# Performance work log

Hardware: AMD Instinct MI355X
Metric: run time of the kernel (lower is better)

## Reference

```python
import jax, jax.numpy as jnp
import numpy as np
from jax import lax

V, E, H, K, T, B = 32000, 512, 512, 32, 256, 64
PAD_W = 0          # word_dict['PAD']
START, END, PAD_L = 30, 31, 0   # label_dict
NEG = -100000.0


def setup_inputs() -> dict:
    key = jax.random.key(0)
    ks = jax.random.split(key, 12)
    s = 1.0 / np.sqrt(H)
    tokens = jax.random.randint(ks[0], (T, B), 1, V, dtype=jnp.int32)   # >PAD_W -> mask all ones
    tags = jax.random.randint(ks[1], (T, B), 1, K - 2, dtype=jnp.int32)
    lengths = jnp.full((B,), T, dtype=jnp.int32)
    embed = jax.random.normal(ks[2], (V, E), jnp.float32) * 0.1
    wih0 = jax.random.uniform(ks[3], (2, 4 * H, E), jnp.float32, -s, s)
    whh0 = jax.random.uniform(ks[4], (2, 4 * H, H), jnp.float32, -s, s)
    b0 = jax.random.uniform(ks[5], (2, 4 * H), jnp.float32, -s, s)
    wih1 = jax.random.uniform(ks[6], (2, 4 * H, 2 * H), jnp.float32, -s, s)
    whh1 = jax.random.uniform(ks[7], (2, 4 * H, H), jnp.float32, -s, s)
    b1 = jax.random.uniform(ks[8], (2, 4 * H), jnp.float32, -s, s)
    lin_w = jax.random.uniform(ks[9], (K, 2 * H), jnp.float32, -s, s)
    lin_b = jax.random.uniform(ks[10], (K,), jnp.float32, -s, s)
    trans = jax.random.normal(ks[11], (K, K), jnp.float32)
    # replicate the torch transition init (same order of assignments)
    trans = trans.at[START, :].set(NEG)
    trans = trans.at[:, END].set(NEG)
    trans = trans.at[:, PAD_L].set(NEG)
    trans = trans.at[PAD_L, :].set(NEG)
    trans = trans.at[PAD_L, END].set(0.0)
    trans = trans.at[PAD_L, PAD_L].set(0.0)
    return dict(tokens=tokens, tags=tags, lengths=lengths, embed=embed,
                wih0=wih0, whh0=whh0, b0=b0, wih1=wih1, whh1=whh1, b1=b1,
                lin_w=lin_w, lin_b=lin_b, trans=trans)


def _lstm_dir(x, w_ih, w_hh, b, reverse):
    # x: [T,B,in] -> hs: [T,B,H]; gates precomputed as one big GEMM
    xp = jnp.einsum('tbi,gi->tbg', x, w_ih) + b  # [T,B,4H]
    h0 = jnp.zeros((x.shape[1], H), x.dtype)

    def step(carry, g_in):
        h, c = carry
        g = g_in + h @ w_hh.T
        i, f, gg, o = jnp.split(g, 4, axis=-1)  # torch gate order i,f,g,o
        c = jax.nn.sigmoid(f) * c + jax.nn.sigmoid(i) * jnp.tanh(gg)
        h = jax.nn.sigmoid(o) * jnp.tanh(c)
        return (h, c), h

    _, hs = lax.scan(step, (h0, h0), xp, reverse=reverse)
    return hs


def _bilstm_layer(x, wih, whh, b):
    return jnp.concatenate([_lstm_dir(x, wih[0], whh[0], b[0], False),
                            _lstm_dir(x, wih[1], whh[1], b[1], True)], axis=-1)


def reference(tokens, tags, lengths, embed, wih0, whh0, b0, wih1, whh1, b1,
              lin_w, lin_b, trans):
    mask = (tokens > PAD_W).astype(jnp.float32)  # [T,B]
    x = embed[tokens]                            # [T,B,E]
    x = _bilstm_layer(x, wih0, whh0, b0)
    x = _bilstm_layer(x, wih1, whh1, b1)
    feats = x @ lin_w.T + lin_b                  # [T,B,K]

    nB = tokens.shape[1]
    # ---- CRF forward algorithm: log Z(x) ----
    init = jnp.full((nB, K), NEG, feats.dtype).at[:, START].set(0.0)

    def step(score, inp):
        emit, m = inp  # [B,K], [B]
        # new[b,k] = logsumexp_j(score[b,j] + trans[k,j]) + emit[b,k]
        new = jax.nn.logsumexp(score[:, None, :] + trans[None, :, :], axis=2) + emit
        return jnp.where(m[:, None] > 0, new, score), None

    z, _ = lax.scan(step, init, (feats, mask))
    log_z = jax.nn.logsumexp(z + trans[END][None, :], axis=1)  # [B]

    # ---- gold path score (vectorized, masked deltas sum) ----
    start_row = jnp.full((1, nB), START, dtype=tags.dtype)
    te = jnp.concatenate([start_row, tags], axis=0)            # [T+1,B]
    trans_s = trans[te[1:], te[:-1]]                           # [T,B]
    emit_s = jnp.take_along_axis(feats, te[1:][..., None].astype(jnp.int32), axis=2)[..., 0]
    gold = jnp.sum(mask * (trans_s + emit_s), axis=0) + trans[END, te[-1]]

    return jnp.sum((log_z - gold) / lengths.astype(jnp.float32))
```

## Files before the change

kernel.cpp:

```cpp
#include <hip/hip_runtime.h>
#include <math.h>

#define T_STEPS 256
#define BATCH   64
#define HID     512
#define KTAGS   32
#define NEGV    -100000.0f
#define START_TAG 30
#define END_TAG   31

#define NBLK      256
#define SPIN_LIM  (1 << 24)
#define LAYER_DONE  300u
#define POISON_DONE 301u
#define POISON    0xFFFFFFFFFFFFFFFFULL

typedef __attribute__((ext_vector_type(8))) short short8;
typedef __attribute__((ext_vector_type(4))) float f32x4;

union V16 { uint4 u; short8 s; };
union HQ  { unsigned long long q[2]; short8 s; };

static __device__ __forceinline__ unsigned short f2b(float f) {
    unsigned u = __float_as_uint(f);
    return (unsigned short)((u + 0x7fffu + ((u >> 16) & 1u)) >> 16);
}
static __device__ __forceinline__ float b2f(unsigned short us) {
    return __uint_as_float(((unsigned)us) << 16);
}

__global__ __launch_bounds__(256) void init_zero(unsigned int* __restrict__ flags,
                                                 unsigned long long* __restrict__ hbuf,
                                                 float* __restrict__ out)
{
    int i = blockIdx.x * 256 + threadIdx.x;
    if (i < 131072)
        __hip_atomic_store(hbuf + i, POISON, __ATOMIC_RELAXED, __HIP_MEMORY_SCOPE_AGENT);
    if (i < 16384)
        __hip_atomic_store(flags + i, 0u, __ATOMIC_RELAXED, __HIP_MEMORY_SCOPE_AGENT);
    if (i == 0)
        __hip_atomic_store(out, 0.0f, __ATOMIC_RELAXED, __HIP_MEMORY_SCOPE_AGENT);
}

__global__ __launch_bounds__(256) void convert_embed(const float* __restrict__ src,
                                                     unsigned short* __restrict__ dst)
{
    long long i = ((long long)blockIdx.x * 256 + threadIdx.x) * 4;
    if (i >= (long long)32000 * 512) return;
    float4 v = *(const float4*)(src + i);
    ushort4 o;
    o.x = f2b(v.x); o.y = f2b(v.y); o.z = f2b(v.z); o.w = f2b(v.w);
    *(ushort4*)(dst + i) = o;
}

__global__ __launch_bounds__(256) void pack_w(const float* __restrict__ wih,
                                              const float* __restrict__ whh,
                                              int xK,
                                              unsigned short* __restrict__ wpack)
{
    const int xKt = xK >> 5, KT = xKt + 16;
    long long t = (long long)blockIdx.x * 256 + threadIdx.x;
    if (t >= (long long)2 * 64 * KT * 2 * 64) return;
    int lane = (int)(t & 63);
    long long rest = t >> 6;
    int nf = (int)(rest & 1); rest >>= 1;
    int kt = (int)(rest % KT); rest /= KT;
    int nt = (int)(rest % 64);
    int d  = (int)(rest / 64);
    int c = lane & 15, q = lane >> 4;
    int bc = nf * 16 + c;
    int r = (bc >> 3) * 512 + nt * 8 + (bc & 7);
    const float* src;
    if (kt < xKt) src = wih + ((long long)d * 2048 * xK + (long long)r * xK + kt * 32 + q * 8);
    else          src = whh + ((long long)d * 2048 * 512 + (long long)r * 512 + (kt - xKt) * 32 + q * 8);
    float4 v0 = *(const float4*)src;
    float4 v1 = *(const float4*)(src + 4);
    unsigned short o[8] = { f2b(v0.x), f2b(v0.y), f2b(v0.z), f2b(v0.w),
                            f2b(v1.x), f2b(v1.y), f2b(v1.z), f2b(v1.w) };
    *(uint4*)(wpack + t * 8) = *(const uint4*)o;
}

template<int XK>
static __device__ __forceinline__ void layer_steps(
    const int d, const int bg, const int nt, const int tid,
    const int* __restrict__ tokens,
    const unsigned short* __restrict__ embB,
    const unsigned short* __restrict__ hs_in,
    const unsigned short* __restrict__ wp,
    const float* __restrict__ bia,
    unsigned short* __restrict__ hso,
    unsigned long long* __restrict__ hbuf64,
    uint4* __restrict__ wlds,
    float (&Gred)[2][4][32][36])
{
    constexpr bool L0  = (XK == 512);
    constexpr int  xKt = XK >> 5;
    constexpr int  KT  = xKt + 16;
    constexpr int  nX  = xKt >> 2;

    const int w = tid >> 6, lane = tid & 63;
    const int lm = lane & 15, q = lane >> 4;
    const int brow = tid >> 3, hc = tid & 7;

    const uint4* wp4 = (const uint4*)wp;
    for (int j = tid; j < KT * 128; j += 256)
        wlds[j] = wp4[j];

    float breg[4];
    #pragma unroll
    for (int g = 0; g < 4; ++g) breg[g] = bia[g * 512 + nt * 8 + hc];
    float creg = 0.0f;

    __syncthreads();

    for (int s = 0; s < T_STEPS; ++s) {
        const int tt = d ? (T_STEPS - 1 - s) : s;
        const int p  = s & 1;

        const unsigned short* xr[2];
        #pragma unroll
        for (int mt = 0; mt < 2; ++mt) {
            int m = mt * 16 + lm;
            if (L0) {
                int tok = tokens[tt * BATCH + bg * 32 + m];
                xr[mt] = embB + (long long)tok * 512;
            } else {
                xr[mt] = hs_in + ((long long)tt * 64 + bg * 32 + m) * 1024;
            }
        }

        uint4 av[nX][2];
        #pragma unroll
        for (int i = 0; i < nX; ++i) {
            const int kt = w * nX + i;
            #pragma unroll
            for (int mt = 0; mt < 2; ++mt)
                av[i][mt] = *(const uint4*)(xr[mt] + kt * 32 + q * 8);
        }

        HQ hq[4][2];
        const unsigned long long* hbq =
            hbuf64 + (long long)(((((s - 1) & 7) * 2 + d) * 2 + bg)) * 4096;
        if (s > 0) {
            #pragma unroll
            for (int i = 0; i < 4; ++i) {
                const int kth = w * 4 + i;
                #pragma unroll
                for (int mt = 0; mt < 2; ++mt) {
                    const int base = (kth * 4 + q) * 64 + (mt * 16 + lm) * 2;
                    hq[i][mt].q[0] = __hip_atomic_load(hbq + base,     __ATOMIC_RELAXED, __HIP_MEMORY_SCOPE_AGENT);
                    hq[i][mt].q[1] = __hip_atomic_load(hbq + base + 1, __ATOMIC_RELAXED, __HIP_MEMORY_SCOPE_AGENT);
                }
            }
        }

        f32x4 acc[2][2];
        #pragma unroll
        for (int mt = 0; mt < 2; ++mt)
            #pragma unroll
            for (int nf = 0; nf < 2; ++nf) acc[mt][nf] = (f32x4)0.0f;

        #pragma unroll
        for (int i = 0; i < nX; ++i) {
            const int kt = w * nX + i;
            V16 a0, a1, b0, b1;
            a0.u = av[i][0]; a1.u = av[i][1];
            b0.u = wlds[(kt * 2 + 0) * 64 + lane];
            b1.u = wlds[(kt * 2 + 1) * 64 + lane];
            acc[0][0] = __builtin_amdgcn_mfma_f32_16x16x32_bf16(a0.s, b0.s, acc[0][0], 0, 0, 0);
            acc[0][1] = __builtin_amdgcn_mfma_f32_16x16x32_bf16(a0.s, b1.s, acc[0][1], 0, 0, 0);
            acc[1][0] = __builtin_amdgcn_mfma_f32_16x16x32_bf16(a1.s, b0.s, acc[1][0], 0, 0, 0);
            acc[1][1] = __builtin_amdgcn_mfma_f32_16x16x32_bf16(a1.s, b1.s, acc[1][1], 0, 0, 0);
        }

        if (s > 0) {
            int pass = 0;
            for (;;) {
                int ok = 1;
                #pragma unroll
                for (int i = 0; i < 4; ++i)
                    #pragma unroll
                    for (int mt = 0; mt < 2; ++mt)
                        ok &= (hq[i][mt].q[0] != POISON) && (hq[i][mt].q[1] != POISON);
                if (__all(ok)) break;
                if (++pass > SPIN_LIM) break;
                if (pass >= 3) __builtin_amdgcn_s_sleep(1);
                #pragma unroll
                for (int i = 0; i < 4; ++i) {
                    const int kth = w * 4 + i;
                    #pragma unroll
                    for (int mt = 0; mt < 2; ++mt) {
                        const int base = (kth * 4 + q) * 64 + (mt * 16 + lm) * 2;
                        hq[i][mt].q[0] = __hip_atomic_load(hbq + base,     __ATOMIC_RELAXED, __HIP_MEMORY_SCOPE_AGENT);
                        hq[i][mt].q[1] = __hip_atomic_load(hbq + base + 1, __ATOMIC_RELAXED, __HIP_MEMORY_SCOPE_AGENT);
                    }
                }
            }

            #pragma unroll
            for (int i = 0; i < 4; ++i) {
                const int kth = w * 4 + i;
                V16 b0, b1;
                b0.u = wlds[((xKt + kth) * 2 + 0) * 64 + lane];
                b1.u = wlds[((xKt + kth) * 2 + 1) * 64 + lane];
                acc[0][0] = __builtin_amdgcn_mfma_f32_16x16x32_bf16(hq[i][0].s, b0.s, acc[0][0], 0, 0, 0);
                acc[0][1] = __builtin_amdgcn_mfma_f32_16x16x32_bf16(hq[i][0].s, b1.s, acc[0][1], 0, 0, 0);
                acc[1][0] = __builtin_amdgcn_mfma_f32_16x16x32_bf16(hq[i][1].s, b0.s, acc[1][0], 0, 0, 0);
                acc[1][1] = __builtin_amdgcn_mfma_f32_16x16x32_bf16(hq[i][1].s, b1.s, acc[1][1], 0, 0, 0);
            }
        }

        #pragma unroll
        for (int mt = 0; mt < 2; ++mt)
            #pragma unroll
            for (int nf = 0; nf < 2; ++nf)
                #pragma unroll
                for (int r = 0; r < 4; ++r) {
                    const int row = mt * 16 + q * 4 + r;
                    const int c   = nf * 16 + lm;
                    const int cp  = (c & 7) * 4 + (c >> 3);
                    Gred[p][w][row][cp] = acc[mt][nf][r];
                }
        __syncthreads();

        float vg[4];
        {
            const float4 g0 = *(const float4*)&Gred[p][0][brow][hc * 4];
            const float4 g1 = *(const float4*)&Gred[p][1][brow][hc * 4];
            const float4 g2 = *(const float4*)&Gred[p][2][brow][hc * 4];
            const float4 g3 = *(const float4*)&Gred[p][3][brow][hc * 4];
            vg[0] = breg[0] + g0.x + g1.x + g2.x + g3.x;
            vg[1] = breg[1] + g0.y + g1.y + g2.y + g3.y;
            vg[2] = breg[2] + g0.z + g1.z + g2.z + g3.z;
            vg[3] = breg[3] + g0.w + g1.w + g2.w + g3.w;
        }
        const float si = 1.0f / (1.0f + __expf(-vg[0]));
        const float sf = 1.0f / (1.0f + __expf(-vg[1]));
        const float so = 1.0f / (1.0f + __expf(-vg[3]));
        const float cn = sf * creg + si * tanhf(vg[2]);
        const float hn = so * tanhf(cn);
        creg = cn;

        unsigned pv = (unsigned)f2b(hn);
        unsigned p2 = pv | (__shfl_xor(pv, 1) << 16);
        unsigned long long hv = (unsigned long long)p2
                              | ((unsigned long long)__shfl_xor(p2, 2) << 32);
        if ((tid & 3) == 0) {
            const int row = brow, cq = hc >> 2;
            unsigned long long* dst =
                hbuf64 + ((long long)((((s & 7) * 2 + d) * 2 + bg) * 64 + nt)) * 64 + row * 2 + cq;
            __hip_atomic_store(dst, hv, __ATOMIC_RELAXED, __HIP_MEMORY_SCOPE_AGENT);
            *(unsigned long long*)(hso + ((long long)tt * 64 + bg * 32 + row) * 1024
                                       + d * 512 + nt * 8 + cq * 4) = hv;
            unsigned long long* pdst =
                hbuf64 + ((long long)(((((s + 2) & 7) * 2 + d) * 2 + bg) * 64 + nt)) * 64 + row * 2 + cq;
            __hip_atomic_store(pdst, POISON, __ATOMIC_RELAXED, __HIP_MEMORY_SCOPE_AGENT);
        }
    }
}

__global__ __launch_bounds__(256, 1) void lstm_mfma(
    const int* __restrict__ tokens,
    const unsigned short* __restrict__ embB,
    const unsigned short* __restrict__ wp0,
    const unsigned short* __restrict__ wp1,
    const float* __restrict__ bb0, const float* __restrict__ bb1,
    unsigned short* __restrict__ hs0,
    unsigned short* __restrict__ hs1,
    unsigned long long* __restrict__ hbuf64,
    unsigned int* __restrict__ flags)
{
    __shared__ uint4 wlds[6144];
    __shared__ __align__(16) float Gred[2][4][32][36];

    const int bid = blockIdx.x;
    const int d   = bid >> 7;
    const int bg  = (bid >> 6) & 1;
    const int nt  = bid & 63;
    const int tid = threadIdx.x;

    layer_steps<512>(d, bg, nt, tid, tokens, embB, (const unsigned short*)nullptr,
                     wp0 + (long long)(d * 64 + nt) * 32 * 1024,
                     bb0 + (long long)d * 2048,
                     hs0, hbuf64, wlds, Gred);

    {
        __threadfence();
        __syncthreads();
        if (tid == 0)
            __hip_atomic_store(flags + bid * 32, LAYER_DONE,
                               __ATOMIC_RELAXED, __HIP_MEMORY_SCOPE_AGENT);
        if (tid < 64) {
            int n = 0;
            for (;;) {
                unsigned a = __hip_atomic_load(flags + tid * 32,         __ATOMIC_RELAXED, __HIP_MEMORY_SCOPE_AGENT);
                unsigned b = __hip_atomic_load(flags + (tid + 64) * 32,  __ATOMIC_RELAXED, __HIP_MEMORY_SCOPE_AGENT);
                unsigned c = __hip_atomic_load(flags + (tid + 128) * 32, __ATOMIC_RELAXED, __HIP_MEMORY_SCOPE_AGENT);
                unsigned e = __hip_atomic_load(flags + (tid + 192) * 32, __ATOMIC_RELAXED, __HIP_MEMORY_SCOPE_AGENT);
                if (__all(a >= LAYER_DONE && b >= LAYER_DONE &&
                          c >= LAYER_DONE && e >= LAYER_DONE)) break;
                __builtin_amdgcn_s_sleep(1);
                if (++n > SPIN_LIM) break;
            }
        }
        __syncthreads();
        if (tid < 64) {
            #pragma unroll
            for (int pp = 0; pp < 8; ++pp) {
                unsigned long long* pd =
                    hbuf64 + ((long long)(((pp * 2 + d) * 2 + bg) * 64 + nt)) * 64 + tid;
                __hip_atomic_store(pd, POISON, __ATOMIC_RELAXED, __HIP_MEMORY_SCOPE_AGENT);
            }
        }
        asm volatile("s_waitcnt vmcnt(0)" ::: "memory");
        __syncthreads();
        if (tid == 0)
            __hip_atomic_store(flags + bid * 32, POISON_DONE,
                               __ATOMIC_RELAXED, __HIP_MEMORY_SCOPE_AGENT);
        if (tid < 64) {
            int n = 0;
            for (;;) {
                unsigned a = __hip_atomic_load(flags + tid * 32,         __ATOMIC_RELAXED, __HIP_MEMORY_SCOPE_AGENT);
                unsigned b = __hip_atomic_load(flags + (tid + 64) * 32,  __ATOMIC_RELAXED, __HIP_MEMORY_SCOPE_AGENT);
                unsigned c = __hip_atomic_load(flags + (tid + 128) * 32, __ATOMIC_RELAXED, __HIP_MEMORY_SCOPE_AGENT);
                unsigned e = __hip_atomic_load(flags + (tid + 192) * 32, __ATOMIC_RELAXED, __HIP_MEMORY_SCOPE_AGENT);
                if (__all(a >= POISON_DONE && b >= POISON_DONE &&
                          c >= POISON_DONE && e >= POISON_DONE)) break;
                __builtin_amdgcn_s_sleep(1);
                if (++n > SPIN_LIM) break;
            }
        }
        __syncthreads();
        __threadfence();
    }

    layer_steps<1024>(d, bg, nt, tid, tokens, embB, hs0,
                      wp1 + (long long)(d * 64 + nt) * 48 * 1024,
                      bb1 + (long long)d * 2048,
                      hs1, hbuf64, wlds, Gred);
}

__global__ __launch_bounds__(256) void gemm_feats(
    const unsigned short* __restrict__ A,
    const float* __restrict__ W,
    const float* __restrict__ bias,
    float* __restrict__ C,
    int M, int N, int K)
{
    __shared__ __align__(16) float As[64][34];
    __shared__ __align__(16) float Ws[32][68];

    const int m0 = blockIdx.y * 64;
    const int tid = threadIdx.x;
    const int tr = tid >> 4;
    const int tc = tid & 15;

    float acc[4][4];
    #pragma unroll
    for (int i = 0; i < 4; ++i)
        #pragma unroll
        for (int j = 0; j < 4; ++j) acc[i][j] = 0.0f;

    for (int k0 = 0; k0 < K; k0 += 32) {
        {
            int row = tid >> 2, g8 = tid & 3;
            uint4 v = *(const uint4*)(A + ((long long)(m0 + row)) * 1024 + k0 + g8 * 8);
            const unsigned short* pv = (const unsigned short*)&v;
            #pragma unroll
            for (int e = 0; e < 8; ++e) As[row][g8 * 8 + e] = b2f(pv[e]);
        }
        {
            int row = tid >> 3, q2 = tid & 7;
            float4 v = *(const float4*)(W + (long long)row * K + k0 + 4 * q2);
            Ws[4*q2+0][row] = v.x; Ws[4*q2+1][row] = v.y;
            Ws[4*q2+2][row] = v.z; Ws[4*q2+3][row] = v.w;
        }
        __syncthreads();
        #pragma unroll 8
        for (int kk = 0; kk < 32; ++kk) {
            float a0 = As[4*tr+0][kk], a1 = As[4*tr+1][kk];
            float a2 = As[4*tr+2][kk], a3 = As[4*tr+3][kk];
            float4 wv = *(const float4*)&Ws[kk][4*tc];
            acc[0][0] += a0*wv.x; acc[0][1] += a0*wv.y; acc[0][2] += a0*wv.z; acc[0][3] += a0*wv.w;
            acc[1][0] += a1*wv.x; acc[1][1] += a1*wv.y; acc[1][2] += a1*wv.z; acc[1][3] += a1*wv.w;
            acc[2][0] += a2*wv.x; acc[2][1] += a2*wv.y; acc[2][2] += a2*wv.z; acc[2][3] += a2*wv.w;
            acc[3][0] += a3*wv.x; acc[3][1] += a3*wv.y; acc[3][2] += a3*wv.z; acc[3][3] += a3*wv.w;
        }
        __syncthreads();
    }
    #pragma unroll
    for (int i = 0; i < 4; ++i) {
        int m = m0 + 4*tr + i;
        #pragma unroll
        for (int j = 0; j < 4; ++j) {
            int n = 4*tc + j;
            if (n < N) C[(long long)m * N + n] = acc[i][j] + bias[n];
        }
    }
}

__global__ __launch_bounds__(1024) void crf_kernel(
    const float* __restrict__ feats,
    const float* __restrict__ trans,
    const int*   __restrict__ tokens,
    const int*   __restrict__ tags,
    const int*   __restrict__ lengths,
    float* __restrict__ out)
{
    const int b = blockIdx.x;
    const int tid = threadIdx.x;
    __shared__ float tr_s[KTAGS*KTAGS];
    __shared__ float score_s[KTAGS];
    __shared__ float emit_s[KTAGS];
    __shared__ float red_s[16];
    __shared__ float logz_s;

    tr_s[tid] = trans[tid];
    if (tid < KTAGS) score_s[tid] = (tid == START_TAG) ? 0.0f : NEGV;
    __syncthreads();

    const int i = tid >> 5, j = tid & 31;
    for (int t = 0; t < T_STEPS; ++t) {
        if (tid < KTAGS) emit_s[tid] = feats[((long long)t*BATCH + b)*KTAGS + tid];
        __syncthreads();
        float e = score_s[j] + tr_s[i*KTAGS + j];
        float m = e;
        m = fmaxf(m, __shfl_xor(m, 1));  m = fmaxf(m, __shfl_xor(m, 2));
        m = fmaxf(m, __shfl_xor(m, 4));  m = fmaxf(m, __shfl_xor(m, 8));
        m = fmaxf(m, __shfl_xor(m, 16));
        float p = __expf(e - m);
        p += __shfl_xor(p, 1); p += __shfl_xor(p, 2); p += __shfl_xor(p, 4);
        p += __shfl_xor(p, 8); p += __shfl_xor(p, 16);
        float nv = m + __logf(p) + emit_s[i];
        int msk = tokens[(long long)t*BATCH + b] > 0;
        __syncthreads();
        if (j == 0) score_s[i] = msk ? nv : score_s[i];
        __syncthreads();
    }

    if (tid < KTAGS) {
        float v = score_s[tid] + tr_s[END_TAG*KTAGS + tid];
        float m = v;
        m = fmaxf(m, __shfl_xor(m, 1));  m = fmaxf(m, __shfl_xor(m, 2));
        m = fmaxf(m, __shfl_xor(m, 4));  m = fmaxf(m, __shfl_xor(m, 8));
        m = fmaxf(m, __shfl_xor(m, 16));
        float p = __expf(v - m);
        p += __shfl_xor(p, 1); p += __shfl_xor(p, 2); p += __shfl_xor(p, 4);
        p += __shfl_xor(p, 8); p += __shfl_xor(p, 16);
        if (tid == 0) logz_s = m + __logf(p);
    }
    __syncthreads();

    float val = 0.0f;
    if (tid < T_STEPS) {
        int t = tid;
        int cur  = tags[(long long)t*BATCH + b];
        int prev = (t == 0) ? START_TAG : tags[(long long)(t-1)*BATCH + b];
        int msk  = tokens[(long long)t*BATCH + b] > 0;
        if (msk) val = tr_s[cur*KTAGS + prev]
                     + feats[((long long)t*BATCH + b)*KTAGS + cur];
    }
    val += __shfl_xor(val, 1);  val += __shfl_xor(val, 2);
    val += __shfl_xor(val, 4);  val += __shfl_xor(val, 8);
    val += __shfl_xor(val, 16); val += __shfl_xor(val, 32);
    int wave = tid >> 6, lane = tid & 63;
    if (lane == 0) red_s[wave] = val;
    __syncthreads();
    if (tid == 0) {
        float g = 0.0f;
        #pragma unroll
        for (int w = 0; w < 16; ++w) g += red_s[w];
        g += tr_s[END_TAG*KTAGS + tags[(long long)(T_STEPS-1)*BATCH + b]];
        atomicAdd(out, (logz_s - g) / (float)lengths[b]);
    }
}

extern "C" void kernel_launch(void* const* d_in, const int* in_sizes, int n_in,
                              void* d_out, int out_size, void* d_ws, size_t ws_size,
                              hipStream_t stream) {
    const int*   tokens  = (const int*)  d_in[0];
    const int*   tags    = (const int*)  d_in[1];
    const int*   lengths = (const int*)  d_in[2];
    const float* embed   = (const float*)d_in[3];
    const float* wih0    = (const float*)d_in[4];
    const float* whh0    = (const float*)d_in[5];
    const float* b0      = (const float*)d_in[6];
    const float* wih1    = (const float*)d_in[7];
    const float* whh1    = (const float*)d_in[8];
    const float* b1      = (const float*)d_in[9];
    const float* lin_w   = (const float*)d_in[10];
    const float* lin_b   = (const float*)d_in[11];
    const float* trans   = (const float*)d_in[12];

    char* ws = (char*)d_ws;
    unsigned short* hs0   = (unsigned short*)(ws);
    unsigned short* hs1   = (unsigned short*)(ws +  33554432ULL);
    unsigned short* embB  = (unsigned short*)(ws +  67108864ULL);
    unsigned short* wp0   = (unsigned short*)(ws +  99876864ULL);
    unsigned short* wp1   = (unsigned short*)(ws + 108265472ULL);
    float*          feats = (float*)        (ws + 120848384ULL);
    unsigned int*   flagsP = (unsigned int*)feats;
    unsigned long long* hbufP = (unsigned long long*)((char*)feats + 65536);

    float* out = (float*)d_out;

    init_zero<<<dim3(512), 256, 0, stream>>>(flagsP, hbufP, out);
    convert_embed<<<dim3(16000), 256, 0, stream>>>(embed, embB);
    pack_w<<<dim3(2048), 256, 0, stream>>>(wih0, whh0, 512,  wp0);
    pack_w<<<dim3(3072), 256, 0, stream>>>(wih1, whh1, 1024, wp1);

    lstm_mfma<<<dim3(NBLK), 256, 0, stream>>>(
        tokens, embB, wp0, wp1, b0, b1, hs0, hs1, hbufP, flagsP);

    gemm_feats<<<dim3(1, 256, 1), 256, 0, stream>>>(
        hs1, lin_w, lin_b, feats, T_STEPS*BATCH, KTAGS, 2*HID);

    crf_kernel<<<dim3(BATCH), 1024, 0, stream>>>(feats, trans, tokens, tags,
                                                 lengths, out);
}
```

Measured before the change: 2.312 ms.

## Process both batch halves per block, halving persistent LSTM grid size

```diff
diff --git a/kernel.cpp b/kernel.cpp
--- a/kernel.cpp
+++ b/kernel.cpp
@@ -9,7 +9,7 @@
 #define START_TAG 30
 #define END_TAG   31
 
-#define NBLK      256
+#define NBLK      128
 #define SPIN_LIM  (1 << 24)
 #define LAYER_DONE  300u
 #define POISON_DONE 301u
@@ -82,7 +82,7 @@
 
 template<int XK>
 static __device__ __forceinline__ void layer_steps(
-    const int d, const int bg, const int nt, const int tid,
+    const int d, const int nt, const int tid,
     const int* __restrict__ tokens,
     const unsigned short* __restrict__ embB,
     const unsigned short* __restrict__ hs_in,
@@ -109,38 +109,32 @@
     float breg[4];
     #pragma unroll
     for (int g = 0; g < 4; ++g) breg[g] = bia[g * 512 + nt * 8 + hc];
-    float creg = 0.0f;
+    float creg0 = 0.0f, creg1 = 0.0f;
 
     __syncthreads();
 
     for (int s = 0; s < T_STEPS; ++s) {
         const int tt = d ? (T_STEPS - 1 - s) : s;
-        const int p  = s & 1;
-
-        const unsigned short* xr[2];
+
+        const unsigned short* xr0[2];
         #pragma unroll
         for (int mt = 0; mt < 2; ++mt) {
             int m = mt * 16 + lm;
-            if (L0) {
-                int tok = tokens[tt * BATCH + bg * 32 + m];
-                xr[mt] = embB + (long long)tok * 512;
-            } else {
-                xr[mt] = hs_in + ((long long)tt * 64 + bg * 32 + m) * 1024;
-            }
-        }
-
-        uint4 av[nX][2];
+            if (L0) xr0[mt] = embB + (long long)tokens[tt * BATCH + m] * 512;
+            else    xr0[mt] = hs_in + ((long long)tt * 64 + m) * 1024;
+        }
+        uint4 av0[nX][2];
         #pragma unroll
         for (int i = 0; i < nX; ++i) {
             const int kt = w * nX + i;
             #pragma unroll
             for (int mt = 0; mt < 2; ++mt)
-                av[i][mt] = *(const uint4*)(xr[mt] + kt * 32 + q * 8);
-        }
-
-        HQ hq[4][2];
-        const unsigned long long* hbq =
-            hbuf64 + (long long)(((((s - 1) & 7) * 2 + d) * 2 + bg)) * 4096;
+                av0[i][mt] = *(const uint4*)(xr0[mt] + kt * 32 + q * 8);
+        }
+
+        HQ hq0[4][2];
+        const unsigned long long* hbq0 =
+            hbuf64 + (long long)((((s - 1) & 7) * 2 + d) * 2 + 0) * 4096;
         if (s > 0) {
             #pragma unroll
             for (int i = 0; i < 4; ++i) {
@@ -148,8 +142,8 @@
                 #pragma unroll
                 for (int mt = 0; mt < 2; ++mt) {
                     const int base = (kth * 4 + q) * 64 + (mt * 16 + lm) * 2;
-                    hq[i][mt].q[0] = __hip_atomic_load(hbq + base,     __ATOMIC_RELAXED, __HIP_MEMORY_SCOPE_AGENT);
-                    hq[i][mt].q[1] = __hip_atomic_load(hbq + base + 1, __ATOMIC_RELAXED, __HIP_MEMORY_SCOPE_AGENT);
+                    hq0[i][mt].q[0] = __hip_atomic_load(hbq0 + base,     __ATOMIC_RELAXED, __HIP_MEMORY_SCOPE_AGENT);
+                    hq0[i][mt].q[1] = __hip_atomic_load(hbq0 + base + 1, __ATOMIC_RELAXED, __HIP_MEMORY_SCOPE_AGENT);
                 }
             }
         }
@@ -164,7 +158,7 @@
         for (int i = 0; i < nX; ++i) {
             const int kt = w * nX + i;
             V16 a0, a1, b0, b1;
-            a0.u = av[i][0]; a1.u = av[i][1];
+            a0.u = av0[i][0]; a1.u = av0[i][1];
             b0.u = wlds[(kt * 2 + 0) * 64 + lane];
             b1.u = wlds[(kt * 2 + 1) * 64 + lane];
             acc[0][0] = __builtin_amdgcn_mfma_f32_16x16x32_bf16(a0.s, b0.s, acc[0][0], 0, 0, 0);
@@ -173,6 +167,37 @@
             acc[1][1] = __builtin_amdgcn_mfma_f32_16x16x32_bf16(a1.s, b1.s, acc[1][1], 0, 0, 0);
         }
 
+        const unsigned short* xr1[2];
+        #pragma unroll
+        for (int mt = 0; mt < 2; ++mt) {
+            int m = mt * 16 + lm;
+            if (L0) xr1[mt] = embB + (long long)tokens[tt * BATCH + 32 + m] * 512;
+            else    xr1[mt] = hs_in + ((long long)tt * 64 + 32 + m) * 1024;
+        }
+        uint4 av1[nX][2];
+        #pragma unroll
+        for (int i = 0; i < nX; ++i) {
+            const int kt = w * nX + i;
+            #pragma unroll
+            for (int mt = 0; mt < 2; ++mt)
+                av1[i][mt] = *(const uint4*)(xr1[mt] + kt * 32 + q * 8);
+        }
+        HQ hq1[4][2];
+        const unsigned long long* hbq1 =
+            hbuf64 + (long long)((((s - 1) & 7) * 2 + d) * 2 + 1) * 4096;
+        if (s > 0) {
+            #pragma unroll
+            for (int i = 0; i < 4; ++i) {
+                const int kth = w * 4 + i;
+                #pragma unroll
+                for (int mt = 0; mt < 2; ++mt) {
+                    const int base = (kth * 4 + q) * 64 + (mt * 16 + lm) * 2;
+                    hq1[i][mt].q[0] = __hip_atomic_load(hbq1 + base,     __ATOMIC_RELAXED, __HIP_MEMORY_SCOPE_AGENT);
+                    hq1[i][mt].q[1] = __hip_atomic_load(hbq1 + base + 1, __ATOMIC_RELAXED, __HIP_MEMORY_SCOPE_AGENT);
+                }
+            }
+        }
+
         if (s > 0) {
             int pass = 0;
             for (;;) {
@@ -181,7 +206,7 @@
                 for (int i = 0; i < 4; ++i)
                     #pragma unroll
                     for (int mt = 0; mt < 2; ++mt)
-                        ok &= (hq[i][mt].q[0] != POISON) && (hq[i][mt].q[1] != POISON);
+                        ok &= (hq0[i][mt].q[0] != POISON) && (hq0[i][mt].q[1] != POISON);
                 if (__all(ok)) break;
                 if (++pass > SPIN_LIM) break;
                 if (pass >= 3) __builtin_amdgcn_s_sleep(1);
@@ -191,22 +216,21 @@
                     #pragma unroll
                     for (int mt = 0; mt < 2; ++mt) {
                         const int base = (kth * 4 + q) * 64 + (mt * 16 + lm) * 2;
-                        hq[i][mt].q[0] = __hip_atomic_load(hbq + base,     __ATOMIC_RELAXED, __HIP_MEMORY_SCOPE_AGENT);
-                        hq[i][mt].q[1] = __hip_atomic_load(hbq + base + 1, __ATOMIC_RELAXED, __HIP_MEMORY_SCOPE_AGENT);
+                        hq0[i][mt].q[0] = __hip_atomic_load(hbq0 + base,     __ATOMIC_RELAXED, __HIP_MEMORY_SCOPE_AGENT);
+                        hq0[i][mt].q[1] = __hip_atomic_load(hbq0 + base + 1, __ATOMIC_RELAXED, __HIP_MEMORY_SCOPE_AGENT);
                     }
                 }
             }
-
             #pragma unroll
             for (int i = 0; i < 4; ++i) {
                 const int kth = w * 4 + i;
                 V16 b0, b1;
                 b0.u = wlds[((xKt + kth) * 2 + 0) * 64 + lane];
                 b1.u = wlds[((xKt + kth) * 2 + 1) * 64 + lane];
-                acc[0][0] = __builtin_amdgcn_mfma_f32_16x16x32_bf16(hq[i][0].s, b0.s, acc[0][0], 0, 0, 0);
-                acc[0][1] = __builtin_amdgcn_mfma_f32_16x16x32_bf16(hq[i][0].s, b1.s, acc[0][1], 0, 0, 0);
-                acc[1][0] = __builtin_amdgcn_mfma_f32_16x16x32_bf16(hq[i][1].s, b0.s, acc[1][0], 0, 0, 0);
-                acc[1][1] = __builtin_amdgcn_mfma_f32_16x16x32_bf16(hq[i][1].s, b1.s, acc[1][1], 0, 0, 0);
+                acc[0][0] = __builtin_amdgcn_mfma_f32_16x16x32_bf16(hq0[i][0].s, b0.s, acc[0][0], 0, 0, 0);
+                acc[0][1] = __builtin_amdgcn_mfma_f32_16x16x32_bf16(hq0[i][0].s, b1.s, acc[0][1], 0, 0, 0);
+                acc[1][0] = __builtin_amdgcn_mfma_f32_16x16x32_bf16(hq0[i][1].s, b0.s, acc[1][0], 0, 0, 0);
+                acc[1][1] = __builtin_amdgcn_mfma_f32_16x16x32_bf16(hq0[i][1].s, b1.s, acc[1][1], 0, 0, 0);
             }
         }
 
@@ -219,42 +243,139 @@
                     const int row = mt * 16 + q * 4 + r;
                     const int c   = nf * 16 + lm;
                     const int cp  = (c & 7) * 4 + (c >> 3);
-                    Gred[p][w][row][cp] = acc[mt][nf][r];
+                    Gred[0][w][row][cp] = acc[mt][nf][r];
                 }
         __syncthreads();
-
-        float vg[4];
         {
-            const float4 g0 = *(const float4*)&Gred[p][0][brow][hc * 4];
-            const float4 g1 = *(const float4*)&Gred[p][1][brow][hc * 4];
-            const float4 g2 = *(const float4*)&Gred[p][2][brow][hc * 4];
-            const float4 g3 = *(const float4*)&Gred[p][3][brow][hc * 4];
-            vg[0] = breg[0] + g0.x + g1.x + g2.x + g3.x;
-            vg[1] = breg[1] + g0.y + g1.y + g2.y + g3.y;
-            vg[2] = breg[2] + g0.z + g1.z + g2.z + g3.z;
-            vg[3] = breg[3] + g0.w + g1.w + g2.w + g3.w;
-        }
-        const float si = 1.0f / (1.0f + __expf(-vg[0]));
-        const float sf = 1.0f / (1.0f + __expf(-vg[1]));
-        const float so = 1.0f / (1.0f + __expf(-vg[3]));
-        const float cn = sf * creg + si * tanhf(vg[2]);
-        const float hn = so * tanhf(cn);
-        creg = cn;
-
-        unsigned pv = (unsigned)f2b(hn);
-        unsigned p2 = pv | (__shfl_xor(pv, 1) << 16);
-        unsigned long long hv = (unsigned long long)p2
-                              | ((unsigned long long)__shfl_xor(p2, 2) << 32);
-        if ((tid & 3) == 0) {
-            const int row = brow, cq = hc >> 2;
-            unsigned long long* dst =
-                hbuf64 + ((long long)((((s & 7) * 2 + d) * 2 + bg) * 64 + nt)) * 64 + row * 2 + cq;
-            __hip_atomic_store(dst, hv, __ATOMIC_RELAXED, __HIP_MEMORY_SCOPE_AGENT);
-            *(unsigned long long*)(hso + ((long long)tt * 64 + bg * 32 + row) * 1024
-                                       + d * 512 + nt * 8 + cq * 4) = hv;
-            unsigned long long* pdst =
-                hbuf64 + ((long long)(((((s + 2) & 7) * 2 + d) * 2 + bg) * 64 + nt)) * 64 + row * 2 + cq;
-            __hip_atomic_store(pdst, POISON, __ATOMIC_RELAXED, __HIP_MEMORY_SCOPE_AGENT);
+            const float4 g0 = *(const float4*)&Gred[0][0][brow][hc * 4];
+            const float4 g1 = *(const float4*)&Gred[0][1][brow][hc * 4];
+            const float4 g2 = *(const float4*)&Gred[0][2][brow][hc * 4];
+            const float4 g3 = *(const float4*)&Gred[0][3][brow][hc * 4];
+            float vg0 = breg[0] + g0.x + g1.x + g2.x + g3.x;
+            float vg1 = breg[1] + g0.y + g1.y + g2.y + g3.y;
+            float vg2 = breg[2] + g0.z + g1.z + g2.z + g3.z;
+            float vg3 = breg[3] + g0.w + g1.w + g2.w + g3.w;
+            const float si = 1.0f / (1.0f + __expf(-vg0));
+            const float sf = 1.0f / (1.0f + __expf(-vg1));
+            const float so = 1.0f / (1.0f + __expf(-vg3));
+            const float cn = sf * creg0 + si * tanhf(vg2);
+            const float hn = so * tanhf(cn);
+            creg0 = cn;
+
+            unsigned pv = (unsigned)f2b(hn);
+            unsigned p2 = pv | (__shfl_xor(pv, 1) << 16);
+            unsigned long long hv = (unsigned long long)p2
+                                  | ((unsigned long long)__shfl_xor(p2, 2) << 32);
+            if ((tid & 3) == 0) {
+                const int row = brow, cq = hc >> 2;
+                unsigned long long* dst =
+                    hbuf64 + ((long long)((((s & 7) * 2 + d) * 2 + 0) * 64 + nt)) * 64 + row * 2 + cq;
+                __hip_atomic_store(dst, hv, __ATOMIC_RELAXED, __HIP_MEMORY_SCOPE_AGENT);
+                *(unsigned long long*)(hso + ((long long)tt * 64 + row) * 1024
+                                           + d * 512 + nt * 8 + cq * 4) = hv;
+                unsigned long long* pdst =
+                    hbuf64 + ((long long)(((((s + 2) & 7) * 2 + d) * 2 + 0) * 64 + nt)) * 64 + row * 2 + cq;
+                __hip_atomic_store(pdst, POISON, __ATOMIC_RELAXED, __HIP_MEMORY_SCOPE_AGENT);
+            }
+        }
+
+        #pragma unroll
+        for (int mt = 0; mt < 2; ++mt)
+            #pragma unroll
+            for (int nf = 0; nf < 2; ++nf) acc[mt][nf] = (f32x4)0.0f;
+
+        #pragma unroll
+        for (int i = 0; i < nX; ++i) {
+            const int kt = w * nX + i;
+            V16 a0, a1, b0, b1;
+            a0.u = av1[i][0]; a1.u = av1[i][1];
+            b0.u = wlds[(kt * 2 + 0) * 64 + lane];
+            b1.u = wlds[(kt * 2 + 1) * 64 + lane];
+            acc[0][0] = __builtin_amdgcn_mfma_f32_16x16x32_bf16(a0.s, b0.s, acc[0][0], 0, 0, 0);
+            acc[0][1] = __builtin_amdgcn_mfma_f32_16x16x32_bf16(a0.s, b1.s, acc[0][1], 0, 0, 0);
+            acc[1][0] = __builtin_amdgcn_mfma_f32_16x16x32_bf16(a1.s, b0.s, acc[1][0], 0, 0, 0);
+            acc[1][1] = __builtin_amdgcn_mfma_f32_16x16x32_bf16(a1.s, b1.s, acc[1][1], 0, 0, 0);
+        }
+
+        if (s > 0) {
+            int pass = 0;
+            for (;;) {
+                int ok = 1;
+                #pragma unroll
+                for (int i = 0; i < 4; ++i)
+                    #pragma unroll
+                    for (int mt = 0; mt < 2; ++mt)
+                        ok &= (hq1[i][mt].q[0] != POISON) && (hq1[i][mt].q[1] != POISON);
+                if (__all(ok)) break;
+                if (++pass > SPIN_LIM) break;
+                if (pass >= 3) __builtin_amdgcn_s_sleep(1);
+                #pragma unroll
+                for (int i = 0; i < 4; ++i) {
+                    const int kth = w * 4 + i;
+                    #pragma unroll
+                    for (int mt = 0; mt < 2; ++mt) {
+                        const int base = (kth * 4 + q) * 64 + (mt * 16 + lm) * 2;
+                        hq1[i][mt].q[0] = __hip_atomic_load(hbq1 + base,     __ATOMIC_RELAXED, __HIP_MEMORY_SCOPE_AGENT);
+                        hq1[i][mt].q[1] = __hip_atomic_load(hbq1 + base + 1, __ATOMIC_RELAXED, __HIP_MEMORY_SCOPE_AGENT);
+                    }
+                }
+            }
+            #pragma unroll
+            for (int i = 0; i < 4; ++i) {
+                const int kth = w * 4 + i;
+                V16 b0, b1;
+                b0.u = wlds[((xKt + kth) * 2 + 0) * 64 + lane];
+                b1.u = wlds[((xKt + kth) * 2 + 1) * 64 + lane];
+                acc[0][0] = __builtin_amdgcn_mfma_f32_16x16x32_bf16(hq1[i][0].s, b0.s, acc[0][0], 0, 0, 0);
+                acc[0][1] = __builtin_amdgcn_mfma_f32_16x16x32_bf16(hq1[i][0].s, b1.s, acc[0][1], 0, 0, 0);
+                acc[1][0] = __builtin_amdgcn_mfma_f32_16x16x32_bf16(hq1[i][1].s, b0.s, acc[1][0], 0, 0, 0);
+                acc[1][1] = __builtin_amdgcn_mfma_f32_16x16x32_bf16(hq1[i][1].s, b1.s, acc[1][1], 0, 0, 0);
+            }
+        }
+
+        #pragma unroll
+        for (int mt = 0; mt < 2; ++mt)
+            #pragma unroll
+            for (int nf = 0; nf < 2; ++nf)
+                #pragma unroll
+                for (int r = 0; r < 4; ++r) {
+                    const int row = mt * 16 + q * 4 + r;
+                    const int c   = nf * 16 + lm;
+                    const int cp  = (c & 7) * 4 + (c >> 3);
+                    Gred[1][w][row][cp] = acc[mt][nf][r];
+                }
+        __syncthreads();
+        {
+            const float4 g0 = *(const float4*)&Gred[1][0][brow][hc * 4];
+            const float4 g1 = *(const float4*)&Gred[1][1][brow][hc * 4];
+            const float4 g2 = *(const float4*)&Gred[1][2][brow][hc * 4];
+            const float4 g3 = *(const float4*)&Gred[1][3][brow][hc * 4];
+            float vg0 = breg[0] + g0.x + g1.x + g2.x + g3.x;
+            float vg1 = breg[1] + g0.y + g1.y + g2.y + g3.y;
+            float vg2 = breg[2] + g0.z + g1.z + g2.z + g3.z;
+            float vg3 = breg[3] + g0.w + g1.w + g2.w + g3.w;
+            const float si = 1.0f / (1.0f + __expf(-vg0));
+            const float sf = 1.0f / (1.0f + __expf(-vg1));
+            const float so = 1.0f / (1.0f + __expf(-vg3));
+            const float cn = sf * creg1 + si * tanhf(vg2);
+            const float hn = so * tanhf(cn);
+            creg1 = cn;
+
+            unsigned pv = (unsigned)f2b(hn);
+            unsigned p2 = pv | (__shfl_xor(pv, 1) << 16);
+            unsigned long long hv = (unsigned long long)p2
+                                  | ((unsigned long long)__shfl_xor(p2, 2) << 32);
+            if ((tid & 3) == 0) {
+                const int row = brow, cq = hc >> 2;
+                unsigned long long* dst =
+                    hbuf64 + ((long long)((((s & 7) * 2 + d) * 2 + 1) * 64 + nt)) * 64 + row * 2 + cq;
+                __hip_atomic_store(dst, hv, __ATOMIC_RELAXED, __HIP_MEMORY_SCOPE_AGENT);
+                *(unsigned long long*)(hso + ((long long)tt * 64 + 32 + row) * 1024
+                                           + d * 512 + nt * 8 + cq * 4) = hv;
+                unsigned long long* pdst =
+                    hbuf64 + ((long long)(((((s + 2) & 7) * 2 + d) * 2 + 1) * 64 + nt)) * 64 + row * 2 + cq;
+                __hip_atomic_store(pdst, POISON, __ATOMIC_RELAXED, __HIP_MEMORY_SCOPE_AGENT);
+            }
         }
     }
 }
@@ -274,12 +395,11 @@
     __shared__ __align__(16) float Gred[2][4][32][36];
 
     const int bid = blockIdx.x;
-    const int d   = bid >> 7;
-    const int bg  = (bid >> 6) & 1;
+    const int d   = bid >> 6;
     const int nt  = bid & 63;
     const int tid = threadIdx.x;
 
-    layer_steps<512>(d, bg, nt, tid, tokens, embB, (const unsigned short*)nullptr,
+    layer_steps<512>(d, nt, tid, tokens, embB, (const unsigned short*)nullptr,
                      wp0 + (long long)(d * 64 + nt) * 32 * 1024,
                      bb0 + (long long)d * 2048,
                      hs0, hbuf64, wlds, Gred);
@@ -293,12 +413,9 @@
         if (tid < 64) {
             int n = 0;
             for (;;) {
-                unsigned a = __hip_atomic_load(flags + tid * 32,         __ATOMIC_RELAXED, __HIP_MEMORY_SCOPE_AGENT);
-                unsigned b = __hip_atomic_load(flags + (tid + 64) * 32,  __ATOMIC_RELAXED, __HIP_MEMORY_SCOPE_AGENT);
-                unsigned c = __hip_atomic_load(flags + (tid + 128) * 32, __ATOMIC_RELAXED, __HIP_MEMORY_SCOPE_AGENT);
-                unsigned e = __hip_atomic_load(flags + (tid + 192) * 32, __ATOMIC_RELAXED, __HIP_MEMORY_SCOPE_AGENT);
-                if (__all(a >= LAYER_DONE && b >= LAYER_DONE &&
-                          c >= LAYER_DONE && e >= LAYER_DONE)) break;
+                unsigned a = __hip_atomic_load(flags + tid * 32,        __ATOMIC_RELAXED, __HIP_MEMORY_SCOPE_AGENT);
+                unsigned b = __hip_atomic_load(flags + (tid + 64) * 32, __ATOMIC_RELAXED, __HIP_MEMORY_SCOPE_AGENT);
+                if (__all(a >= LAYER_DONE && b >= LAYER_DONE)) break;
                 __builtin_amdgcn_s_sleep(1);
                 if (++n > SPIN_LIM) break;
             }
@@ -307,9 +424,12 @@
         if (tid < 64) {
             #pragma unroll
             for (int pp = 0; pp < 8; ++pp) {
-                unsigned long long* pd =
-                    hbuf64 + ((long long)(((pp * 2 + d) * 2 + bg) * 64 + nt)) * 64 + tid;
-                __hip_atomic_store(pd, POISON, __ATOMIC_RELAXED, __HIP_MEMORY_SCOPE_AGENT);
+                #pragma unroll
+                for (int bg = 0; bg < 2; ++bg) {
+                    unsigned long long* pd =
+                        hbuf64 + ((long long)(((pp * 2 + d) * 2 + bg) * 64 + nt)) * 64 + tid;
+                    __hip_atomic_store(pd, POISON, __ATOMIC_RELAXED, __HIP_MEMORY_SCOPE_AGENT);
+                }
             }
         }
         asm volatile("s_waitcnt vmcnt(0)" ::: "memory");
@@ -320,12 +440,9 @@
         if (tid < 64) {
             int n = 0;
             for (;;) {
-                unsigned a = __hip_atomic_load(flags + tid * 32,         __ATOMIC_RELAXED, __HIP_MEMORY_SCOPE_AGENT);
-                unsigned b = __hip_atomic_load(flags + (tid + 64) * 32,  __ATOMIC_RELAXED, __HIP_MEMORY_SCOPE_AGENT);
-                unsigned c = __hip_atomic_load(flags + (tid + 128) * 32, __ATOMIC_RELAXED, __HIP_MEMORY_SCOPE_AGENT);
-                unsigned e = __hip_atomic_load(flags + (tid + 192) * 32, __ATOMIC_RELAXED, __HIP_MEMORY_SCOPE_AGENT);
-                if (__all(a >= POISON_DONE && b >= POISON_DONE &&
-                          c >= POISON_DONE && e >= POISON_DONE)) break;
+                unsigned a = __hip_atomic_load(flags + tid * 32,        __ATOMIC_RELAXED, __HIP_MEMORY_SCOPE_AGENT);
+                unsigned b = __hip_atomic_load(flags + (tid + 64) * 32, __ATOMIC_RELAXED, __HIP_MEMORY_SCOPE_AGENT);
+                if (__all(a >= POISON_DONE && b >= POISON_DONE)) break;
                 __builtin_amdgcn_s_sleep(1);
                 if (++n > SPIN_LIM) break;
             }
@@ -334,7 +451,7 @@
         __threadfence();
     }
 
-    layer_steps<1024>(d, bg, nt, tid, tokens, embB, hs0,
+    layer_steps<1024>(d, nt, tid, tokens, embB, hs0,
                       wp1 + (long long)(d * 64 + nt) * 48 * 1024,
                       bb1 + (long long)d * 2048,
                       hs1, hbuf64, wlds, Gred);
```

Result: slower. 3.837 ms (+66.0%).
